# Kernel optimization log

Hardware: AMD Instinct MI355X
Metric: run time of the kernel (lower is better)

## Reference

```python
import jax, jax.numpy as jnp
import numpy as np

B, S, H, NH = 2, 2048, 1024, 16
D = H // NH
EPS = 1.1920929e-07  # torch fp32 finfo eps used by F.rms_norm default
ROPE_BASE = 10000.0


def setup_inputs() -> dict:
    key = jax.random.key(0)
    k0, k1, k2, k3 = jax.random.split(key, 4)
    return {
        "x": jax.random.normal(k0, (B, S, H), jnp.float32),
        "ve": jax.random.normal(k1, (B, S, H), jnp.float32),
        "W_qkv": jax.random.normal(k2, (3 * H, H), jnp.float32) * 0.02,
        "W_o": jax.random.normal(k3, (H, H), jnp.float32) * 0.02,
        "lambdas": jnp.array([0.5, 0.5], jnp.float32),
    }


def _rms_norm(x):
    # F.rms_norm without learnable weight, over last dim
    return x * jax.lax.rsqrt(jnp.mean(x * x, axis=-1, keepdims=True) + EPS)


def _rope(x):
    # x: [b, s, h, d]; rotate-half style RoPE matching the Rotary module
    d = x.shape[-1]
    inv_freq = (1.0 / ROPE_BASE) ** (jnp.arange(0, d, 2, dtype=jnp.float32) / d)
    t = jnp.arange(x.shape[1], dtype=jnp.float32)
    freqs = t[:, None] * inv_freq[None, :]          # [s, d/2]
    cos = jnp.cos(freqs)[None, :, None, :]
    sin = jnp.sin(freqs)[None, :, None, :]
    x1, x2 = jnp.split(x, 2, axis=-1)
    return jnp.concatenate([x1 * cos + x2 * sin, -x1 * sin + x2 * cos], axis=-1)


def reference(x, ve, W_qkv, W_o, lambdas):
    qkv = x @ W_qkv.T                                # [b, s, 3H]
    q, k, v = jnp.split(qkv, 3, axis=-1)
    rs = lambda a: a.reshape(B, S, NH, D)            # b s (h d) -> b s h d
    q, k, v = rs(q), rs(k), rs(v)
    q = _rope(_rms_norm(q))
    k = _rope(_rms_norm(k))
    v = lambdas[0] * v + lambdas[1] * rs(ve)         # value-lambda mix
    scale = 1.0 / jnp.sqrt(jnp.asarray(D, jnp.float32))  # flex_attention default
    scores = jnp.einsum('bqhd,bkhd->bhqk', q, k) * scale
    causal = jnp.tril(jnp.ones((S, S), bool))
    scores = jnp.where(causal[None, None], scores, jnp.asarray(-jnp.inf, scores.dtype))
    p = jax.nn.softmax(scores, axis=-1)
    a = jnp.einsum('bhqk,bkhd->bqhd', p, v).reshape(B, S, H)
    return a @ W_o.T
```

## Files before the change

### kernel.cpp

```cpp
#include <hip/hip_runtime.h>
#include <math.h>

typedef __bf16 bf16;
typedef __attribute__((ext_vector_type(8))) __bf16 bf16x8;
typedef __attribute__((ext_vector_type(4))) __bf16 bf16x4;
typedef __attribute__((ext_vector_type(4))) float f32x4;

#define B_  2
#define S_  2048
#define H_  1024
#define NH_ 16
#define D_  64

__device__ __forceinline__ f32x4 mfma16(bf16x8 a, bf16x8 b, f32x4 c) {
    return __builtin_amdgcn_mfma_f32_16x16x32_bf16(a, b, c, 0, 0, 0);
}

__device__ __forceinline__ void async16(void* lds, const void* g) {
    __builtin_amdgcn_global_load_lds(
        (const __attribute__((address_space(1))) unsigned int*)g,
        (__attribute__((address_space(3))) unsigned int*)lds, 16, 0, 0);
}

__global__ __launch_bounds__(256) void cvt_main(
    const float* __restrict__ x, const float* __restrict__ wqkv,
    bf16* __restrict__ xb, bf16* __restrict__ wqb, float2* __restrict__ tab)
{
    const int bid = blockIdx.x, tid = threadIdx.x;
    if (bid < 4096) {
        int i = bid * 256 + tid;
        f32x4 v = *(const f32x4*)(x + (size_t)i * 4);
        bf16x4 o; o[0]=(bf16)v[0]; o[1]=(bf16)v[1]; o[2]=(bf16)v[2]; o[3]=(bf16)v[3];
        *(bf16x4*)(xb + (size_t)i * 4) = o;
    } else if (bid < 7168) {
        int i = (bid - 4096) * 256 + tid;
        f32x4 v = *(const f32x4*)(wqkv + (size_t)i * 4);
        bf16x4 o; o[0]=(bf16)v[0]; o[1]=(bf16)v[1]; o[2]=(bf16)v[2]; o[3]=(bf16)v[3];
        *(bf16x4*)(wqb + (size_t)i * 4) = o;
    } else {
        int idx = (bid - 7168) * 256 + tid;
        int s = idx >> 5, i = idx & 31;
        float f = exp2f((float)i * (-13.287712379549449f / 32.0f));
        float sn, cs;
        sincosf((float)s * f, &sn, &cs);
        tab[idx] = make_float2(cs, sn);
    }
}

__global__ __launch_bounds__(256) void cvt_bf16(const float* __restrict__ src,
                                                bf16* __restrict__ dst, int n4) {
    int i = blockIdx.x * 256 + threadIdx.x;
    if (i >= n4) return;
    f32x4 v = *(const f32x4*)(src + (size_t)i * 4);
    bf16x4 o; o[0]=(bf16)v[0]; o[1]=(bf16)v[1]; o[2]=(bf16)v[2]; o[3]=(bf16)v[3];
    *(bf16x4*)(dst + (size_t)i * 4) = o;
}

template <int EPI, int NT>
__global__ __launch_bounds__(256) void gemm_bt(
    const bf16* __restrict__ A, const bf16* __restrict__ W,
    int M, int N, int K,
    float* __restrict__ outF,
    bf16* __restrict__ qb, bf16* __restrict__ kb, bf16* __restrict__ vtb,
    const float* __restrict__ ve, const float* __restrict__ lambdas,
    const float2* __restrict__ tab)
{
    constexpr int JN = NT / 32;
    __shared__ bf16 Al[128][64];
    __shared__ bf16 Bl[NT][64];
    const int m0   = blockIdx.y * 128;
    const int n0   = blockIdx.x * NT;
    const int tid  = threadIdx.x;
    const int lane = tid & 63;
    const int w    = tid >> 6;
    const int quad = lane >> 4;
    const int l16  = lane & 15;
    const int wm   = (w >> 1) * 64;
    const int wn   = (w & 1) * (NT / 2);
    const int r8   = lane >> 3;
    const int cs   = ((lane & 7) ^ r8) * 8;

    const f32x4 Z4 = {0.f, 0.f, 0.f, 0.f};
    f32x4 acc[4][JN];
#pragma unroll
    for (int i = 0; i < 4; ++i)
#pragma unroll
        for (int j = 0; j < JN; ++j) acc[i][j] = Z4;

    for (int k0 = 0; k0 < K; k0 += 64) {
        {
            const bf16* gA = A + (size_t)(m0 + w * 32 + r8) * K + k0 + cs;
            async16(&Al[w * 32][0],      gA);
            async16(&Al[w * 32 + 8][0],  gA + (size_t)8  * K);
            async16(&Al[w * 32 + 16][0], gA + (size_t)16 * K);
            async16(&Al[w * 32 + 24][0], gA + (size_t)24 * K);
        }
        if constexpr (NT == 128) {
            const bf16* gB = W + (size_t)(n0 + w * 32 + r8) * K + k0 + cs;
            async16(&Bl[w * 32][0],      gB);
            async16(&Bl[w * 32 + 8][0],  gB + (size_t)8  * K);
            async16(&Bl[w * 32 + 16][0], gB + (size_t)16 * K);
            async16(&Bl[w * 32 + 24][0], gB + (size_t)24 * K);
        } else {
            const bf16* gB = W + (size_t)(n0 + w * 16 + r8) * K + k0 + cs;
            async16(&Bl[w * 16][0],     gB);
            async16(&Bl[w * 16 + 8][0], gB + (size_t)8 * K);
        }
        __syncthreads();
#pragma unroll
        for (int ks = 0; ks < 2; ++ks) {
            bf16x8 af[4], bfg[JN];
#pragma unroll
            for (int i = 0; i < 4; ++i)
                af[i] = *(const bf16x8*)
                    &Al[wm + i * 16 + l16][(((ks << 2) + quad) ^ (l16 & 7)) * 8];
#pragma unroll
            for (int j = 0; j < JN; ++j)
                bfg[j] = *(const bf16x8*)
                    &Bl[wn + j * 16 + l16][(((ks << 2) + quad) ^ (l16 & 7)) * 8];
#pragma unroll
            for (int i = 0; i < 4; ++i)
#pragma unroll
                for (int j = 0; j < JN; ++j)
                    acc[i][j] = mfma16(af[i], bfg[j], acc[i][j]);
        }
        __syncthreads();
    }

    if constexpr (EPI == 1) {
#pragma unroll
        for (int i = 0; i < 4; ++i)
#pragma unroll
            for (int j = 0; j < JN; ++j)
#pragma unroll
                for (int r = 0; r < 4; ++r) {
                    int m = m0 + wm + i * 16 + quad * 4 + r;
                    int n = n0 + wn + j * 16 + l16;
                    outF[(size_t)m * N + n] = acc[i][j][r];
                }
    } else {
        const int nbase = n0 + wn;
        const int which = nbase >> 10;
        const int h     = (nbase & (H_ - 1)) >> 6;
        if (which < 2) {
            bf16* dst = which ? kb : qb;
#pragma unroll
            for (int i = 0; i < 4; ++i) {
                float ss[4];
#pragma unroll
                for (int r = 0; r < 4; ++r)
                    ss[r] = acc[i][0][r] * acc[i][0][r] + acc[i][1][r] * acc[i][1][r]
                          + acc[i][2][r] * acc[i][2][r] + acc[i][3][r] * acc[i][3][r];
#pragma unroll
                for (int r = 0; r < 4; ++r) {
                    ss[r] += __shfl_xor(ss[r], 1);
                    ss[r] += __shfl_xor(ss[r], 2);
                    ss[r] += __shfl_xor(ss[r], 4);
                    ss[r] += __shfl_xor(ss[r], 8);
                }
#pragma unroll
                for (int r = 0; r < 4; ++r) {
                    int    m   = m0 + wm + i * 16 + quad * 4 + r;
                    int    bb  = m >> 11, s = m & (S_ - 1);
                    float  rms = rsqrtf(ss[r] * (1.0f / 64.0f) + 1.1920929e-07f);
                    float  x0 = acc[i][0][r] * rms, x1 = acc[i][1][r] * rms;
                    float  x2 = acc[i][2][r] * rms, x3 = acc[i][3][r] * rms;
                    float2 t0 = tab[(size_t)s * 32 + l16];
                    float2 t1 = tab[(size_t)s * 32 + 16 + l16];
                    bf16*  bp = dst + ((size_t)(bb * NH_ + h) * S_ + s) * D_;
                    bp[l16]      = (bf16)(x0 * t0.x + x2 * t0.y);
                    bp[16 + l16] = (bf16)(x1 * t1.x + x3 * t1.y);
                    bp[32 + l16] = (bf16)(x2 * t0.x - x0 * t0.y);
                    bp[48 + l16] = (bf16)(x3 * t1.x - x1 * t1.y);
                }
            }
        } else {
            const float l0 = lambdas[0], l1 = lambdas[1];
#pragma unroll
            for (int i = 0; i < 4; ++i) {
                const int m00 = m0 + wm + i * 16 + quad * 4;
                const int bb  = m00 >> 11, s = m00 & (S_ - 1);
#pragma unroll
                for (int j = 0; j < 4; ++j) {
                    const int d = j * 16 + l16;
                    bf16x4 pk;
#pragma unroll
                    for (int r = 0; r < 4; ++r) {
                        float vm = l0 * acc[i][j][r]
                                 + l1 * ve[(size_t)(m00 + r) * H_ + h * 64 + d];
                        pk[r] = (bf16)vm;
                    }
                    *(bf16x4*)&vtb[((size_t)(bb * NH_ + h) * D_ + d) * S_ + s] = pk;
                }
            }
        }
    }
}

__global__ __launch_bounds__(256) void attn(
    const bf16* __restrict__ Q, const bf16* __restrict__ Kg,
    const bf16* __restrict__ Vt, bf16* __restrict__ Og)
{
    __shared__ bf16 Kl[2][64][64];
    __shared__ bf16 Vl[2][64][64];
    __shared__ bf16 Pl[4][16][64];

    const int bh   = blockIdx.y;
    const int b    = bh >> 4;
    const int h    = bh & 15;
    const int tid  = threadIdx.x;
    const int lane = tid & 63;
    const int w    = tid >> 6;
    const int quad = lane >> 4;
    const int l16  = lane & 15;
    const int l7   = l16 & 7;

    const bf16* Qp = Q  + (size_t)bh * S_ * D_;
    const bf16* Kp = Kg + (size_t)bh * S_ * D_;
    const bf16* Vp = Vt + (size_t)bh * D_ * S_;

    const int srow = lane >> 3;
    const int schk = (lane & 7) ^ (lane >> 3);
    const f32x4 Z4 = {0.f, 0.f, 0.f, 0.f};
    const float C1 = 0.18033688011112042f;
    const float C2 = -11.541560327111707f;

    auto stage = [&](int p, int kb0) {
        const bf16* gK = Kp + (size_t)(kb0 + w * 16 + srow) * D_ + schk * 8;
        async16(&Kl[p][w * 16][0], gK);
        async16(&Kl[p][w * 16 + 8][0], gK + (size_t)8 * D_);
        const bf16* gV = Vp + (size_t)(w * 16 + srow) * S_ + kb0 + schk * 8;
        async16(&Vl[p][w * 16][0], gV);
        async16(&Vl[p][w * 16 + 8][0], gV + (size_t)8 * S_);
    };

    for (int half = 0; half < 2; ++half) {
        const int qt    = half ? (31 - blockIdx.x) : blockIdx.x;
        const int qbase = qt * 64 + w * 16;
        const int qi    = qbase + l16;

        bf16x8 qf0 = *(const bf16x8*)(Qp + (size_t)(qbase + l16) * D_ + quad * 8);
        bf16x8 qf1 = *(const bf16x8*)(Qp + (size_t)(qbase + l16) * D_ + 32 + quad * 8);

        f32x4 of[4];
#pragma unroll
        for (int dt = 0; dt < 4; ++dt) of[dt] = Z4;
        float lsum = 0.f;

        const int nch = qt + 1;
        __syncthreads();
        stage(0, 0);
        for (int c = 0; c < nch; ++c) {
            const int p   = c & 1;
            const int kb0 = c * 64;
            __syncthreads();
            if (c + 1 < nch) stage(p ^ 1, kb0 + 64);

            float ps = 0.f;
            if (c < qt) {
#pragma unroll
                for (int nt = 0; nt < 4; ++nt) {
                    bf16x8 kf0 = *(const bf16x8*)&Kl[p][nt * 16 + l16][(quad ^ l7) * 8];
                    bf16x8 kf1 = *(const bf16x8*)&Kl[p][nt * 16 + l16][((quad + 4) ^ l7) * 8];
                    f32x4 sacc = Z4;
                    sacc = mfma16(kf0, qf0, sacc);
                    sacc = mfma16(kf1, qf1, sacc);
                    bf16x4 pk;
#pragma unroll
                    for (int r = 0; r < 4; ++r) {
                        float pv = exp2f(fmaf(sacc[r], C1, C2));
                        ps += pv;
                        pk[r] = (bf16)pv;
                    }
                    *(bf16x4*)&Pl[w][l16][((nt * 2 + (quad >> 1)) ^ l7) * 8 + (quad & 1) * 4] = pk;
                }
            } else {
#pragma unroll
                for (int nt = 0; nt < 4; ++nt) {
                    bf16x8 kf0 = *(const bf16x8*)&Kl[p][nt * 16 + l16][(quad ^ l7) * 8];
                    bf16x8 kf1 = *(const bf16x8*)&Kl[p][nt * 16 + l16][((quad + 4) ^ l7) * 8];
                    f32x4 sacc = Z4;
                    sacc = mfma16(kf0, qf0, sacc);
                    sacc = mfma16(kf1, qf1, sacc);
                    bf16x4 pk;
#pragma unroll
                    for (int r = 0; r < 4; ++r) {
                        int   key = kb0 + nt * 16 + quad * 4 + r;
                        float pv  = (key <= qi) ? exp2f(fmaf(sacc[r], C1, C2)) : 0.f;
                        ps += pv;
                        pk[r] = (bf16)pv;
                    }
                    *(bf16x4*)&Pl[w][l16][((nt * 2 + (quad >> 1)) ^ l7) * 8 + (quad & 1) * 4] = pk;
                }
            }
            ps += __shfl_xor(ps, 16);
            ps += __shfl_xor(ps, 32);
            lsum += ps;

            bf16x8 pf0 = *(const bf16x8*)&Pl[w][l16][(quad ^ l7) * 8];
            bf16x8 pf1 = *(const bf16x8*)&Pl[w][l16][((quad + 4) ^ l7) * 8];
#pragma unroll
            for (int dt = 0; dt < 4; ++dt) {
                bf16x8 vf0 = *(const bf16x8*)&Vl[p][dt * 16 + l16][(quad ^ l7) * 8];
                bf16x8 vf1 = *(const bf16x8*)&Vl[p][dt * 16 + l16][((quad + 4) ^ l7) * 8];
                of[dt] = mfma16(pf0, vf0, of[dt]);
                of[dt] = mfma16(pf1, vf1, of[dt]);
            }
        }

#pragma unroll
        for (int r = 0; r < 4; ++r) {
            float ld = __shfl(lsum, quad * 4 + r);
            float rl = 1.0f / ld;
            int   qq = qbase + quad * 4 + r;
#pragma unroll
            for (int dt = 0; dt < 4; ++dt)
                Og[((size_t)(b * S_ + qq)) * H_ + h * D_ + dt * 16 + l16] =
                    (bf16)(of[dt][r] * rl);
        }
    }
}

extern "C" void kernel_launch(void* const* d_in, const int* in_sizes, int n_in,
                              void* d_out, int out_size, void* d_ws, size_t ws_size,
                              hipStream_t stream)
{
    const float* x       = (const float*)d_in[0];
    const float* ve      = (const float*)d_in[1];
    const float* Wqkv    = (const float*)d_in[2];
    const float* Wo      = (const float*)d_in[3];
    const float* lambdas = (const float*)d_in[4];
    float* out = (float*)d_out;

    char* od = (char*)d_out;
    char* ws = (char*)d_ws;
    const size_t MB = 1024 * 1024;
    bf16*   xb  = (bf16*)(od);
    bf16*   wqb = (bf16*)(od + 8 * MB);
    float2* tab = (float2*)(od + 14 * MB);
    bf16*   qb  = (bf16*)(ws);
    bf16*   kb  = (bf16*)(ws + 8 * MB);
    bf16*   vtb = (bf16*)(ws + 16 * MB);
    bf16*   ao  = (bf16*)(ws + 24 * MB);
    bf16*   wob = (bf16*)(ws);

    cvt_main<<<7424, 256, 0, stream>>>(x, Wqkv, xb, wqb, tab);
    gemm_bt<0, 128><<<dim3(24, 32), 256, 0, stream>>>(
        xb, wqb, B_ * S_, 3 * H_, H_, nullptr, qb, kb, vtb, ve, lambdas, (const float2*)tab);
    attn<<<dim3(16, B_ * NH_), 256, 0, stream>>>(qb, kb, vtb, ao);
    cvt_bf16<<<1024, 256, 0, stream>>>(Wo, wob, (H_ * H_) / 4);
    gemm_bt<1, 64><<<dim3(16, 32), 256, 0, stream>>>(
        ao, wob, B_ * S_, H_, H_, out, nullptr, nullptr, nullptr, nullptr, nullptr, nullptr);
}
```

Baseline: 209.4 us.

## Add dedicated 256x256 double-buffered QKV GEMM with staged prefetch interleaving

Replaces the generic 128x128 QKV projection GEMM with a dedicated 512-thread kernel that computes 256x256 tiles. It double-buffers LDS and prefetches the next K-slice in quarter chunks interleaved with MFMA phases, using split barriers and s_setprio. The aim is to hide global-load latency and raise data reuse per tile, cutting LDS traffic per FLOP. The trade-offs are higher register pressure (128 accumulator floats per thread), 128KB of LDS per block, and only 192 blocks for the whole GPU, which may underfill the CUs.

New measurement: 208.7 us. No clear change (-0.3%).

```diff
diff --git a/kernel.cpp b/kernel.cpp
--- a/kernel.cpp
+++ b/kernel.cpp
@@ -56,14 +56,194 @@
     *(bf16x4*)(dst + (size_t)i * 4) = o;
 }
 
+__global__ __launch_bounds__(512, 2) void gemm_qkv(
+    const bf16* __restrict__ A, const bf16* __restrict__ W,
+    bf16* __restrict__ qb, bf16* __restrict__ kb, bf16* __restrict__ vtb,
+    const float* __restrict__ ve, const float* __restrict__ lambdas,
+    const float2* __restrict__ tab)
+{
+    constexpr int K  = H_;
+    constexpr int NS = K >> 6;
+    __shared__ bf16 Al[2][256][64];
+    __shared__ bf16 Bl[2][256][64];
+    const int m0   = blockIdx.y * 256;
+    const int n0   = blockIdx.x * 256;
+    const int tid  = threadIdx.x;
+    const int lane = tid & 63;
+    const int w    = tid >> 6;
+    const int quad = lane >> 4;
+    const int l16  = lane & 15;
+    const int l7r  = l16 & 7;
+    const int wm   = (w >> 2) * 128;
+    const int wn   = (w & 3) * 64;
+    const int r8   = lane >> 3;
+    const int cs   = ((lane & 7) ^ r8) * 8;
+
+    auto stage_half = [&](int sl, int kt, int h) {
+        const int k0 = kt << 6;
+        if (h < 2) {
+            const bf16* g = A + (size_t)(m0 + h * 128 + w * 16 + r8) * K + k0 + cs;
+            async16(&Al[sl][h * 128 + w * 16][0],     g);
+            async16(&Al[sl][h * 128 + w * 16 + 8][0], g + (size_t)8 * K);
+        } else {
+            const bf16* g = W + (size_t)(n0 + (h - 2) * 128 + w * 16 + r8) * K + k0 + cs;
+            async16(&Bl[sl][(h - 2) * 128 + w * 16][0],     g);
+            async16(&Bl[sl][(h - 2) * 128 + w * 16 + 8][0], g + (size_t)8 * K);
+        }
+    };
+
+    const f32x4 Z4 = {0.f, 0.f, 0.f, 0.f};
+    f32x4 acc[8][4];
+#pragma unroll
+    for (int i = 0; i < 8; ++i)
+#pragma unroll
+        for (int j = 0; j < 4; ++j) acc[i][j] = Z4;
+
+    stage_half(0, 0, 0); stage_half(0, 0, 1); stage_half(0, 0, 2); stage_half(0, 0, 3);
+    stage_half(1, (NS > 1 ? 1 : 0), 0);
+
+    for (int t = 0; t < NS; ++t) {
+        const int cur = t & 1;
+        const int kt1 = (t + 1 < NS) ? t + 1 : NS - 1;
+        const int kt2 = (t + 2 < NS) ? t + 2 : NS - 1;
+        bf16x8 aL[4][2], aH[4][2], bq0[2][2], bq1[2][2];
+
+        asm volatile("s_waitcnt vmcnt(2)" ::: "memory");
+        __builtin_amdgcn_s_barrier();
+#pragma unroll
+        for (int ks = 0; ks < 2; ++ks) {
+#pragma unroll
+            for (int i = 0; i < 4; ++i)
+                aL[i][ks] = *(const bf16x8*)
+                    &Al[cur][wm + i * 16 + l16][(((ks << 2) + quad) ^ l7r) * 8];
+#pragma unroll
+            for (int j = 0; j < 2; ++j)
+                bq0[j][ks] = *(const bf16x8*)
+                    &Bl[cur][wn + j * 16 + l16][(((ks << 2) + quad) ^ l7r) * 8];
+        }
+        stage_half(cur ^ 1, kt1, 1);
+        __builtin_amdgcn_s_setprio(1);
+#pragma unroll
+        for (int ks = 0; ks < 2; ++ks)
+#pragma unroll
+            for (int i = 0; i < 4; ++i)
+#pragma unroll
+                for (int j = 0; j < 2; ++j)
+                    acc[i][j] = mfma16(aL[i][ks], bq0[j][ks], acc[i][j]);
+        __builtin_amdgcn_s_setprio(0);
+
+        __builtin_amdgcn_s_barrier();
+#pragma unroll
+        for (int ks = 0; ks < 2; ++ks)
+#pragma unroll
+            for (int j = 0; j < 2; ++j)
+                bq1[j][ks] = *(const bf16x8*)
+                    &Bl[cur][wn + 32 + j * 16 + l16][(((ks << 2) + quad) ^ l7r) * 8];
+        stage_half(cur ^ 1, kt1, 2);
+        __builtin_amdgcn_s_setprio(1);
+#pragma unroll
+        for (int ks = 0; ks < 2; ++ks)
+#pragma unroll
+            for (int i = 0; i < 4; ++i)
+#pragma unroll
+                for (int j = 0; j < 2; ++j)
+                    acc[i][2 + j] = mfma16(aL[i][ks], bq1[j][ks], acc[i][2 + j]);
+        __builtin_amdgcn_s_setprio(0);
+
+        __builtin_amdgcn_s_barrier();
+#pragma unroll
+        for (int ks = 0; ks < 2; ++ks)
+#pragma unroll
+            for (int i = 0; i < 4; ++i)
+                aH[i][ks] = *(const bf16x8*)
+                    &Al[cur][wm + 64 + i * 16 + l16][(((ks << 2) + quad) ^ l7r) * 8];
+        stage_half(cur ^ 1, kt1, 3);
+        __builtin_amdgcn_s_setprio(1);
+#pragma unroll
+        for (int ks = 0; ks < 2; ++ks)
+#pragma unroll
+            for (int i = 0; i < 4; ++i)
+#pragma unroll
+                for (int j = 0; j < 2; ++j)
+                    acc[4 + i][j] = mfma16(aH[i][ks], bq0[j][ks], acc[4 + i][j]);
+        __builtin_amdgcn_s_setprio(0);
+
+        __builtin_amdgcn_s_barrier();
+        stage_half(cur, kt2, 0);
+        __builtin_amdgcn_s_setprio(1);
+#pragma unroll
+        for (int ks = 0; ks < 2; ++ks)
+#pragma unroll
+            for (int i = 0; i < 4; ++i)
+#pragma unroll
+                for (int j = 0; j < 2; ++j)
+                    acc[4 + i][2 + j] = mfma16(aH[i][ks], bq1[j][ks], acc[4 + i][2 + j]);
+        __builtin_amdgcn_s_setprio(0);
+    }
+    asm volatile("s_waitcnt vmcnt(0)" ::: "memory");
+
+    const int nbase = n0 + wn;
+    const int which = nbase >> 10;
+    const int h     = (nbase & (H_ - 1)) >> 6;
+    if (which < 2) {
+        bf16* dst = which ? kb : qb;
+#pragma unroll
+        for (int i = 0; i < 8; ++i) {
+            float ss[4];
+#pragma unroll
+            for (int r = 0; r < 4; ++r)
+                ss[r] = acc[i][0][r] * acc[i][0][r] + acc[i][1][r] * acc[i][1][r]
+                      + acc[i][2][r] * acc[i][2][r] + acc[i][3][r] * acc[i][3][r];
+#pragma unroll
+            for (int r = 0; r < 4; ++r) {
+                ss[r] += __shfl_xor(ss[r], 1);
+                ss[r] += __shfl_xor(ss[r], 2);
+                ss[r] += __shfl_xor(ss[r], 4);
+                ss[r] += __shfl_xor(ss[r], 8);
+            }
+#pragma unroll
+            for (int r = 0; r < 4; ++r) {
+                int    m   = m0 + wm + i * 16 + quad * 4 + r;
+                int    bb  = m >> 11, s = m & (S_ - 1);
+                float  rms = rsqrtf(ss[r] * (1.0f / 64.0f) + 1.1920929e-07f);
+                float  x0 = acc[i][0][r] * rms, x1 = acc[i][1][r] * rms;
+                float  x2 = acc[i][2][r] * rms, x3 = acc[i][3][r] * rms;
+                float2 t0 = tab[(size_t)s * 32 + l16];
+                float2 t1 = tab[(size_t)s * 32 + 16 + l16];
+                bf16*  bp = dst + ((size_t)(bb * NH_ + h) * S_ + s) * D_;
+                bp[l16]      = (bf16)(x0 * t0.x + x2 * t0.y);
+                bp[16 + l16] = (bf16)(x1 * t1.x + x3 * t1.y);
+                bp[32 + l16] = (bf16)(x2 * t0.x - x0 * t0.y);
+                bp[48 + l16] = (bf16)(x3 * t1.x - x1 * t1.y);
+            }
+        }
+    } else {
+        const float l0 = lambdas[0], l1 = lambdas[1];
+#pragma unroll
+        for (int i = 0; i < 8; ++i) {
+            const int m00 = m0 + wm + i * 16 + quad * 4;
+            const int bb  = m00 >> 11, s = m00 & (S_ - 1);
+#pragma unroll
+            for (int j = 0; j < 4; ++j) {
+                const int d = j * 16 + l16;
+                bf16x4 pk;
+#pragma unroll
+                for (int r = 0; r < 4; ++r) {
+                    float vm = l0 * acc[i][j][r]
+                             + l1 * ve[(size_t)(m00 + r) * H_ + h * 64 + d];
+                    pk[r] = (bf16)vm;
+                }
+                *(bf16x4*)&vtb[((size_t)(bb * NH_ + h) * D_ + d) * S_ + s] = pk;
+            }
+        }
+    }
+}
+
 template <int EPI, int NT>
 __global__ __launch_bounds__(256) void gemm_bt(
     const bf16* __restrict__ A, const bf16* __restrict__ W,
     int M, int N, int K,
-    float* __restrict__ outF,
-    bf16* __restrict__ qb, bf16* __restrict__ kb, bf16* __restrict__ vtb,
-    const float* __restrict__ ve, const float* __restrict__ lambdas,
-    const float2* __restrict__ tab)
+    float* __restrict__ outF)
 {
     constexpr int JN = NT / 32;
     __shared__ bf16 Al[128][64];
@@ -95,13 +275,7 @@
             async16(&Al[w * 32 + 16][0], gA + (size_t)16 * K);
             async16(&Al[w * 32 + 24][0], gA + (size_t)24 * K);
         }
-        if constexpr (NT == 128) {
-            const bf16* gB = W + (size_t)(n0 + w * 32 + r8) * K + k0 + cs;
-            async16(&Bl[w * 32][0],      gB);
-            async16(&Bl[w * 32 + 8][0],  gB + (size_t)8  * K);
-            async16(&Bl[w * 32 + 16][0], gB + (size_t)16 * K);
-            async16(&Bl[w * 32 + 24][0], gB + (size_t)24 * K);
-        } else {
+        {
             const bf16* gB = W + (size_t)(n0 + w * 16 + r8) * K + k0 + cs;
             async16(&Bl[w * 16][0],     gB);
             async16(&Bl[w * 16 + 8][0], gB + (size_t)8 * K);
@@ -127,74 +301,16 @@
         __syncthreads();
     }
 
-    if constexpr (EPI == 1) {
-#pragma unroll
-        for (int i = 0; i < 4; ++i)
-#pragma unroll
-            for (int j = 0; j < JN; ++j)
-#pragma unroll
-                for (int r = 0; r < 4; ++r) {
-                    int m = m0 + wm + i * 16 + quad * 4 + r;
-                    int n = n0 + wn + j * 16 + l16;
-                    outF[(size_t)m * N + n] = acc[i][j][r];
-                }
-    } else {
-        const int nbase = n0 + wn;
-        const int which = nbase >> 10;
-        const int h     = (nbase & (H_ - 1)) >> 6;
-        if (which < 2) {
-            bf16* dst = which ? kb : qb;
-#pragma unroll
-            for (int i = 0; i < 4; ++i) {
-                float ss[4];
-#pragma unroll
-                for (int r = 0; r < 4; ++r)
-                    ss[r] = acc[i][0][r] * acc[i][0][r] + acc[i][1][r] * acc[i][1][r]
-                          + acc[i][2][r] * acc[i][2][r] + acc[i][3][r] * acc[i][3][r];
-#pragma unroll
-                for (int r = 0; r < 4; ++r) {
-                    ss[r] += __shfl_xor(ss[r], 1);
-                    ss[r] += __shfl_xor(ss[r], 2);
-                    ss[r] += __shfl_xor(ss[r], 4);
-                    ss[r] += __shfl_xor(ss[r], 8);
-                }
-#pragma unroll
-                for (int r = 0; r < 4; ++r) {
-                    int    m   = m0 + wm + i * 16 + quad * 4 + r;
-                    int    bb  = m >> 11, s = m & (S_ - 1);
-                    float  rms = rsqrtf(ss[r] * (1.0f / 64.0f) + 1.1920929e-07f);
-                    float  x0 = acc[i][0][r] * rms, x1 = acc[i][1][r] * rms;
-                    float  x2 = acc[i][2][r] * rms, x3 = acc[i][3][r] * rms;
-                    float2 t0 = tab[(size_t)s * 32 + l16];
-                    float2 t1 = tab[(size_t)s * 32 + 16 + l16];
-                    bf16*  bp = dst + ((size_t)(bb * NH_ + h) * S_ + s) * D_;
-                    bp[l16]      = (bf16)(x0 * t0.x + x2 * t0.y);
-                    bp[16 + l16] = (bf16)(x1 * t1.x + x3 * t1.y);
-                    bp[32 + l16] = (bf16)(x2 * t0.x - x0 * t0.y);
-                    bp[48 + l16] = (bf16)(x3 * t1.x - x1 * t1.y);
-                }
-            }
-        } else {
-            const float l0 = lambdas[0], l1 = lambdas[1];
-#pragma unroll
-            for (int i = 0; i < 4; ++i) {
-                const int m00 = m0 + wm + i * 16 + quad * 4;
-                const int bb  = m00 >> 11, s = m00 & (S_ - 1);
-#pragma unroll
-                for (int j = 0; j < 4; ++j) {
-                    const int d = j * 16 + l16;
-                    bf16x4 pk;
-#pragma unroll
-                    for (int r = 0; r < 4; ++r) {
-                        float vm = l0 * acc[i][j][r]
-                                 + l1 * ve[(size_t)(m00 + r) * H_ + h * 64 + d];
-                        pk[r] = (bf16)vm;
-                    }
-                    *(bf16x4*)&vtb[((size_t)(bb * NH_ + h) * D_ + d) * S_ + s] = pk;
-                }
-            }
-        }
-    }
+#pragma unroll
+    for (int i = 0; i < 4; ++i)
+#pragma unroll
+        for (int j = 0; j < JN; ++j)
+#pragma unroll
+            for (int r = 0; r < 4; ++r) {
+                int m = m0 + wm + i * 16 + quad * 4 + r;
+                int n = n0 + wn + j * 16 + l16;
+                outF[(size_t)m * N + n] = acc[i][j][r];
+            }
 }
 
 __global__ __launch_bounds__(256) void attn(
@@ -345,10 +461,10 @@
     bf16*   wob = (bf16*)(ws);
 
     cvt_main<<<7424, 256, 0, stream>>>(x, Wqkv, xb, wqb, tab);
-    gemm_bt<0, 128><<<dim3(24, 32), 256, 0, stream>>>(
-        xb, wqb, B_ * S_, 3 * H_, H_, nullptr, qb, kb, vtb, ve, lambdas, (const float2*)tab);
+    gemm_qkv<<<dim3(12, 16), 512, 0, stream>>>(
+        xb, wqb, qb, kb, vtb, ve, lambdas, (const float2*)tab);
     attn<<<dim3(16, B_ * NH_), 256, 0, stream>>>(qb, kb, vtb, ao);
     cvt_bf16<<<1024, 256, 0, stream>>>(Wo, wob, (H_ * H_) / 4);
     gemm_bt<1, 64><<<dim3(16, 32), 256, 0, stream>>>(
-        ao, wob, B_ * S_, H_, H_, out, nullptr, nullptr, nullptr, nullptr, nullptr, nullptr);
-}
+        ao, wob, B_ * S_, H_, H_, out);
+}
```
